# Kernel tuning notes

Measured on AMD Instinct MI355X. Metric: run time of the kernel, lower is better.

The kernel has to match this reference:

```python
import jax, jax.numpy as jnp
import numpy as np

N = 50000        # nodes
E = 300000       # edges (before self-loops)
F_IN = 128       # input feature dim
H = 2            # attention heads
D = 128          # per-head dim (hidden_dim/heads)
C = 3            # output classes
G = 64           # graphs in batch
NEG_SLOPE = 0.2  # PyG GATConv default leaky-relu slope


def setup_inputs() -> dict:
    key = jax.random.key(0)
    ks = jax.random.split(key, 9)
    x = jax.random.normal(ks[0], (N, F_IN), jnp.float32)
    edge_index = jax.random.randint(ks[1], (2, E), 0, N, dtype=jnp.int64)
    batch = jnp.sort(jax.random.randint(ks[2], (N,), 0, G, dtype=jnp.int64))
    W = jax.random.normal(ks[3], (F_IN, H, D), jnp.float32) * 0.05   # GAT lin weight
    att_src = jax.random.normal(ks[4], (H, D), jnp.float32) * 0.1
    att_dst = jax.random.normal(ks[5], (H, D), jnp.float32) * 0.1
    bias_gat = jax.random.normal(ks[6], (H * D,), jnp.float32) * 0.01
    fc_w = jax.random.normal(ks[7], (H * D, C), jnp.float32) * 0.05
    fc_b = jax.random.normal(ks[8], (C,), jnp.float32) * 0.01
    a = jnp.array(1.0, jnp.float32)
    return dict(x=x, edge_index=edge_index, batch=batch, W=W, att_src=att_src,
                att_dst=att_dst, bias_gat=bias_gat, fc_w=fc_w, fc_b=fc_b, a=a)


def reference(x, edge_index, batch, W, att_src, att_dst, bias_gat, fc_w, fc_b, a):
    n = x.shape[0]
    # PyG GATConv adds self-loops by default
    loops = jnp.arange(n, dtype=edge_index.dtype)
    src = jnp.concatenate([edge_index[0], loops])   # message sources j
    tgt = jnp.concatenate([edge_index[1], loops])   # message targets i

    xw = jnp.einsum('nf,nfhd->nhd', x[:, :, None, None] * 0 + x[:, :, None, None], W[None]) if False else jnp.einsum('nf,fhd->nhd', x, W)  # [N,H,D]
    a_s = jnp.sum(xw * att_src, axis=-1)            # [N,H]
    a_d = jnp.sum(xw * att_dst, axis=-1)            # [N,H]

    e = a_s[src] + a_d[tgt]                         # [E+N,H]
    e = jnp.where(e > 0, e, NEG_SLOPE * e)          # leaky relu
    # segment softmax over incoming edges of each target node
    m = jax.ops.segment_max(e, tgt, num_segments=n)
    ex = jnp.exp(e - m[tgt])
    denom = jax.ops.segment_sum(ex, tgt, num_segments=n)
    alpha = ex / denom[tgt]                         # [E+N,H]

    out = jax.ops.segment_sum(alpha[:, :, None] * xw[src], tgt, num_segments=n)  # [N,H,D]
    z = out.reshape(n, H * D) + bias_gat
    z = jax.nn.relu(z)
    z = z @ fc_w + fc_b                              # [N,C]
    z = jax.nn.log_softmax(z, axis=1)
    z = jax.ops.segment_sum(z, batch, num_segments=G)  # global_add_pool -> [G,C]
    z = a * z
    return jax.nn.log_softmax(z, axis=1)
```

## Files before the change

### kernel.cpp

```cpp
#include <hip/hip_runtime.h>
#include <hip/hip_bf16.h>

typedef __hip_bfloat16 bf16;
typedef __attribute__((ext_vector_type(8))) short bf16x8;
typedef __attribute__((ext_vector_type(4))) float f32x4;

#define F_IN    128
#define HD      256
#define N_C     3
#define N_G     64
#define NEG_SLOPE 0.2f
#define NPART   512
#define DMAX    32

__device__ __forceinline__ float b2f(unsigned short u) {
    return __uint_as_float(((unsigned int)u) << 16);
}
__device__ __forceinline__ unsigned short f2bs(float f) {
    unsigned int u = __float_as_uint(f);
    return (unsigned short)((u + 0x7FFFu + ((u >> 16) & 1u)) >> 16);
}

__global__ void scatter_kernel(const int* __restrict__ ei, int* __restrict__ cnt,
                               int* __restrict__ ssrc32,
                               const float* __restrict__ W,
                               unsigned short* __restrict__ WTf, int e) {
    int i = blockIdx.x * blockDim.x + threadIdx.x;
    if (i < HD * F_IN) {
        int j = i & 7;
        int L = (i >> 3) & 63;
        int c = (i >> 9) & 3;
        int t = i >> 11;
        int f  = c * 32 + (L >> 4) * 8 + j;
        int hd = t * 16 + (L & 15);
        WTf[i] = f2bs(W[f * HD + hd]);
    }
    if (i < e) {
        int s = ei[i];
        int t = ei[e + i];
        int p = atomicAdd(&cnt[t], 1);
        if (p < DMAX) ssrc32[(size_t)t * DMAX + p] = s;
    }
}

__global__ __launch_bounds__(256) void xw_mfma_kernel(const float* __restrict__ x,
                                                      const uint4* __restrict__ WTf,
                                                      bf16* __restrict__ xw,
                                                      const float* __restrict__ att_src,
                                                      const float* __restrict__ att_dst,
                                                      float* __restrict__ asd, int n) {
    __shared__ uint4 wt_lds[4096];
    int tid = threadIdx.x;
    int wid = tid >> 6, lane = tid & 63;
    int r16 = lane & 15, quad = lane >> 4;
    int rb = blockIdx.x * 64 + wid * 16;
    bool valid = rb < n;
    int rbl = valid ? rb : 0;

    const float* xr = x + (size_t)(rbl + r16) * F_IN + quad * 8;
    float4 f0a = *(const float4*)(xr + 0);
    float4 f1a = *(const float4*)(xr + 4);
    float4 f0b = *(const float4*)(xr + 32);
    float4 f1b = *(const float4*)(xr + 36);
    float4 f0c = *(const float4*)(xr + 64);
    float4 f1c = *(const float4*)(xr + 68);
    float4 f0d = *(const float4*)(xr + 96);
    float4 f1d = *(const float4*)(xr + 100);

    #pragma unroll
    for (int r = 0; r < 16; r++)
        wt_lds[r * 256 + tid] = WTf[r * 256 + tid];

    bf16x8 xf[4];
    {
        bf16x8 a;
        a[0]=(short)f2bs(f0a.x); a[1]=(short)f2bs(f0a.y); a[2]=(short)f2bs(f0a.z); a[3]=(short)f2bs(f0a.w);
        a[4]=(short)f2bs(f1a.x); a[5]=(short)f2bs(f1a.y); a[6]=(short)f2bs(f1a.z); a[7]=(short)f2bs(f1a.w);
        xf[0]=a;
        a[0]=(short)f2bs(f0b.x); a[1]=(short)f2bs(f0b.y); a[2]=(short)f2bs(f0b.z); a[3]=(short)f2bs(f0b.w);
        a[4]=(short)f2bs(f1b.x); a[5]=(short)f2bs(f1b.y); a[6]=(short)f2bs(f1b.z); a[7]=(short)f2bs(f1b.w);
        xf[1]=a;
        a[0]=(short)f2bs(f0c.x); a[1]=(short)f2bs(f0c.y); a[2]=(short)f2bs(f0c.z); a[3]=(short)f2bs(f0c.w);
        a[4]=(short)f2bs(f1c.x); a[5]=(short)f2bs(f1c.y); a[6]=(short)f2bs(f1c.z); a[7]=(short)f2bs(f1c.w);
        xf[2]=a;
        a[0]=(short)f2bs(f0d.x); a[1]=(short)f2bs(f0d.y); a[2]=(short)f2bs(f0d.z); a[3]=(short)f2bs(f0d.w);
        a[4]=(short)f2bs(f1d.x); a[5]=(short)f2bs(f1d.y); a[6]=(short)f2bs(f1d.z); a[7]=(short)f2bs(f1d.w);
        xf[3]=a;
    }
    __syncthreads();

    const unsigned short* wls = (const unsigned short*)wt_lds;
    float s0a = 0.f, s1a = 0.f, d0a = 0.f, d1a = 0.f;
    for (int t = 0; t < 16; t++) {
        f32x4 acc = {0.f, 0.f, 0.f, 0.f};
        #pragma unroll
        for (int c = 0; c < 4; c++) {
            bf16x8 wf = *(const bf16x8*)(wls + ((t * 4 + c) * 64 + lane) * 8);
            acc = __builtin_amdgcn_mfma_f32_16x16x32_bf16(wf, xf[c], acc, 0, 0, 0);
        }
        int colbase = t * 16;
        float4 as4 = *(const float4*)(att_src + colbase + quad * 4);
        float4 ad4 = *(const float4*)(att_dst + colbase + quad * 4);
        if (valid) {
            unsigned int w0 = (unsigned int)f2bs(acc[0]) | ((unsigned int)f2bs(acc[1]) << 16);
            unsigned int w1 = (unsigned int)f2bs(acc[2]) | ((unsigned int)f2bs(acc[3]) << 16);
            *(uint2*)((unsigned short*)xw + (size_t)(rb + r16) * HD + colbase + quad * 4)
                = make_uint2(w0, w1);
        }
        float ds = acc[0]*as4.x + acc[1]*as4.y + acc[2]*as4.z + acc[3]*as4.w;
        float dd = acc[0]*ad4.x + acc[1]*ad4.y + acc[2]*ad4.z + acc[3]*ad4.w;
        if (t < 8) { s0a += ds; d0a += dd; }
        else       { s1a += ds; d1a += dd; }
    }

    #pragma unroll
    for (int o = 16; o <= 32; o <<= 1) {
        s0a += __shfl_xor(s0a, o, 64);
        s1a += __shfl_xor(s1a, o, 64);
        d0a += __shfl_xor(d0a, o, 64);
        d1a += __shfl_xor(d1a, o, 64);
    }
    if (valid && quad == 0) {
        float4 v;
        v.x = s0a; v.y = s1a; v.z = d0a; v.w = d1a;
        ((float4*)asd)[rb + r16] = v;
    }
}

__global__ __launch_bounds__(256) void main_kernel(const bf16* __restrict__ xw,
                                                   const float* __restrict__ asd,
                                                   const int* __restrict__ cnt,
                                                   const int* __restrict__ ssrc32,
                                                   const int* __restrict__ batch,
                                                   const float* __restrict__ bias,
                                                   const float* __restrict__ fcw,
                                                   const float* __restrict__ fcb,
                                                   float* __restrict__ gsumP, int n) {
    __shared__ int   sidx[4][64];
    __shared__ float salp[4][2][64];
    int wid = threadIdx.x >> 6, lane = threadIdx.x & 63;
    int head = lane >> 5;
    int node = blockIdx.x * 4 + wid;
    if (node >= n) return;

    float4 my = ((const float4*)asd)[node];
    float ad0 = my.z, ad1 = my.w;
    int dege = cnt[node];
    if (dege > DMAX) dege = DMAX;
    int deg = dege + 1;
    const int* srow = ssrc32 + (size_t)node * DMAX;

    float a0 = 0.f, a1 = 0.f, a2 = 0.f, a3 = 0.f;

    bool act = lane < deg;
    int myidx = node;
    float e0 = -1e30f, e1 = -1e30f;
    if (lane < dege) {
        myidx = srow[lane];
        float4 sa = ((const float4*)asd)[myidx];
        e0 = sa.x + ad0;
        e1 = sa.y + ad1;
    } else if (lane == dege) {
        e0 = my.x + ad0;
        e1 = my.y + ad1;
    }
    e0 = (e0 > 0.f) ? e0 : NEG_SLOPE * e0;
    e1 = (e1 > 0.f) ? e1 : NEG_SLOPE * e1;
    if (!act) { e0 = -1e30f; e1 = -1e30f; }

    float m0 = e0, m1 = e1;
    #pragma unroll
    for (int o = 1; o <= 8; o <<= 1) {
        m0 = fmaxf(m0, __shfl_xor(m0, o, 64));
        m1 = fmaxf(m1, __shfl_xor(m1, o, 64));
    }
    if (deg > 16) {
        #pragma unroll
        for (int o = 16; o <= 32; o <<= 1) {
            m0 = fmaxf(m0, __shfl_xor(m0, o, 64));
            m1 = fmaxf(m1, __shfl_xor(m1, o, 64));
        }
    }
    float al0 = act ? __expf(e0 - m0) : 0.f;
    float al1 = act ? __expf(e1 - m1) : 0.f;
    float s0 = al0, s1 = al1;
    #pragma unroll
    for (int o = 1; o <= 8; o <<= 1) {
        s0 += __shfl_xor(s0, o, 64);
        s1 += __shfl_xor(s1, o, 64);
    }
    if (deg > 16) {
        #pragma unroll
        for (int o = 16; o <= 32; o <<= 1) {
            s0 += __shfl_xor(s0, o, 64);
            s1 += __shfl_xor(s1, o, 64);
        }
    }
    if (act) {
        sidx[wid][lane] = myidx;
        salp[wid][0][lane] = al0 / s0;
        salp[wid][1][lane] = al1 / s1;
    }

    int e = 0;
    for (; e + 4 <= deg; e += 4) {
        int i0 = sidx[wid][e + 0], i1 = sidx[wid][e + 1];
        int i2 = sidx[wid][e + 2], i3 = sidx[wid][e + 3];
        ushort4 v0 = ((const ushort4*)(xw + (size_t)i0 * HD))[lane];
        ushort4 v1 = ((const ushort4*)(xw + (size_t)i1 * HD))[lane];
        ushort4 v2 = ((const ushort4*)(xw + (size_t)i2 * HD))[lane];
        ushort4 v3 = ((const ushort4*)(xw + (size_t)i3 * HD))[lane];
        float w0 = salp[wid][head][e + 0];
        float w1 = salp[wid][head][e + 1];
        float w2 = salp[wid][head][e + 2];
        float w3 = salp[wid][head][e + 3];
        a0 += w0 * b2f(v0.x) + w1 * b2f(v1.x) + w2 * b2f(v2.x) + w3 * b2f(v3.x);
        a1 += w0 * b2f(v0.y) + w1 * b2f(v1.y) + w2 * b2f(v2.y) + w3 * b2f(v3.y);
        a2 += w0 * b2f(v0.z) + w1 * b2f(v1.z) + w2 * b2f(v2.z) + w3 * b2f(v3.z);
        a3 += w0 * b2f(v0.w) + w1 * b2f(v1.w) + w2 * b2f(v2.w) + w3 * b2f(v3.w);
    }
    for (; e < deg; e++) {
        int i0 = sidx[wid][e];
        ushort4 v0 = ((const ushort4*)(xw + (size_t)i0 * HD))[lane];
        float w0 = salp[wid][head][e];
        a0 += w0 * b2f(v0.x); a1 += w0 * b2f(v0.y);
        a2 += w0 * b2f(v0.z); a3 += w0 * b2f(v0.w);
    }

    float4 bv = ((const float4*)bias)[lane];
    float z0 = fmaxf(a0 + bv.x, 0.f);
    float z1 = fmaxf(a1 + bv.y, 0.f);
    float z2 = fmaxf(a2 + bv.z, 0.f);
    float z3 = fmaxf(a3 + bv.w, 0.f);

    const float* fp = fcw + lane * 12;
    float4 c0 = *(const float4*)(fp);
    float4 c1 = *(const float4*)(fp + 4);
    float4 c2 = *(const float4*)(fp + 8);
    float l0 = z0 * c0.x + z1 * c0.w + z2 * c1.z + z3 * c2.y;
    float l1 = z0 * c0.y + z1 * c1.x + z2 * c1.w + z3 * c2.z;
    float l2 = z0 * c0.z + z1 * c1.y + z2 * c2.x + z3 * c2.w;
    #pragma unroll
    for (int o = 32; o > 0; o >>= 1) {
        l0 += __shfl_xor(l0, o, 64);
        l1 += __shfl_xor(l1, o, 64);
        l2 += __shfl_xor(l2, o, 64);
    }
    if (lane == 0) {
        l0 += fcb[0]; l1 += fcb[1]; l2 += fcb[2];
        float m = fmaxf(l0, fmaxf(l1, l2));
        float lse = m + __logf(__expf(l0 - m) + __expf(l1 - m) + __expf(l2 - m));
        int b = batch[node];
        int part = node & (NPART - 1);
        atomicAdd(&gsumP[(b * 3 + 0) * NPART + part], l0 - lse);
        atomicAdd(&gsumP[(b * 3 + 1) * NPART + part], l1 - lse);
        atomicAdd(&gsumP[(b * 3 + 2) * NPART + part], l2 - lse);
    }
}

__global__ __launch_bounds__(64) void final_kernel(const float* __restrict__ gsumP,
                                                   const float* __restrict__ a,
                                                   float* __restrict__ out) {
    int g = blockIdx.x;
    int lane = threadIdx.x;
    float v[3];
    #pragma unroll
    for (int c = 0; c < 3; c++) {
        float s = 0.f;
        for (int p = lane; p < NPART; p += 64)
            s += gsumP[(g * 3 + c) * NPART + p];
        #pragma unroll
        for (int o = 32; o > 0; o >>= 1) s += __shfl_xor(s, o, 64);
        v[c] = s;
    }
    if (lane == 0) {
        float av = a[0];
        float v0 = v[0] * av, v1 = v[1] * av, v2 = v[2] * av;
        float m = fmaxf(v0, fmaxf(v1, v2));
        float lse = m + __logf(__expf(v0 - m) + __expf(v1 - m) + __expf(v2 - m));
        out[g * 3 + 0] = v0 - lse;
        out[g * 3 + 1] = v1 - lse;
        out[g * 3 + 2] = v2 - lse;
    }
}

extern "C" void kernel_launch(void* const* d_in, const int* in_sizes, int n_in,
                              void* d_out, int out_size, void* d_ws, size_t ws_size,
                              hipStream_t stream) {
    const float* x       = (const float*)d_in[0];
    const int*   ei      = (const int*)d_in[1];
    const int*   batch   = (const int*)d_in[2];
    const float* W       = (const float*)d_in[3];
    const float* att_src = (const float*)d_in[4];
    const float* att_dst = (const float*)d_in[5];
    const float* bias    = (const float*)d_in[6];
    const float* fcw     = (const float*)d_in[7];
    const float* fcb     = (const float*)d_in[8];
    const float* a_scale = (const float*)d_in[9];
    float* out = (float*)d_out;

    const int n = in_sizes[2];
    const int e = in_sizes[1] / 2;

    char* ws = (char*)d_ws;
    bf16*  xw     = (bf16*)ws;
    float* asd    = (float*)(ws + 25600000);
    int*   cnt    = (int*)(ws + 26400000);
    float* gsumP  = (float*)(ws + 26600000);
    int*   ssrc32 = (int*)(ws + 26993216);
    unsigned short* WTf = (unsigned short*)(ws + 33393216);

    int eb256 = (e + 255) / 256;

    hipMemsetAsync(cnt, 0, (size_t)n * 4 + (size_t)N_G * N_C * NPART * 4, stream);

    hipLaunchKernelGGL(scatter_kernel, dim3(eb256), dim3(256), 0, stream,
                       ei, cnt, ssrc32, W, WTf, e);
    hipLaunchKernelGGL(xw_mfma_kernel, dim3((n + 63) / 64), dim3(256), 0, stream,
                       x, (const uint4*)WTf, xw, att_src, att_dst, asd, n);
    hipLaunchKernelGGL(main_kernel,    dim3((n + 3) / 4), dim3(256), 0, stream,
                       xw, asd, cnt, ssrc32, batch, bias, fcw, fcb, gsumP, n);
    hipLaunchKernelGGL(final_kernel,   dim3(N_G), dim3(64), 0, stream, gsumP, a_scale, out);
}
```

Baseline: 165.9 us.

## Fuse final pooling into main kernel, batch gathers by eight, vectorize edge scatter

```diff
diff --git a/kernel.cpp b/kernel.cpp
--- a/kernel.cpp
+++ b/kernel.cpp
@@ -35,11 +35,16 @@
         int hd = t * 16 + (L & 15);
         WTf[i] = f2bs(W[f * HD + hd]);
     }
-    if (i < e) {
-        int s = ei[i];
-        int t = ei[e + i];
-        int p = atomicAdd(&cnt[t], 1);
-        if (p < DMAX) ssrc32[(size_t)t * DMAX + p] = s;
+    int i2 = i * 2;
+    if (i2 < e) {
+        int2 s2 = *(const int2*)(ei + i2);
+        int2 t2 = *(const int2*)(ei + e + i2);
+        int p = atomicAdd(&cnt[t2.x], 1);
+        if (p < DMAX) ssrc32[(size_t)t2.x * DMAX + p] = s2.x;
+        if (i2 + 1 < e) {
+            p = atomicAdd(&cnt[t2.y], 1);
+            if (p < DMAX) ssrc32[(size_t)t2.y * DMAX + p] = s2.y;
+        }
     }
 }
 
@@ -135,152 +140,154 @@
                                                    const float* __restrict__ bias,
                                                    const float* __restrict__ fcw,
                                                    const float* __restrict__ fcb,
-                                                   float* __restrict__ gsumP, int n) {
+                                                   float* __restrict__ gsumP,
+                                                   const float* __restrict__ a_scale,
+                                                   float* __restrict__ out,
+                                                   int* __restrict__ done, int n) {
     __shared__ int   sidx[4][64];
     __shared__ float salp[4][2][64];
+    __shared__ int   islast;
     int wid = threadIdx.x >> 6, lane = threadIdx.x & 63;
     int head = lane >> 5;
     int node = blockIdx.x * 4 + wid;
-    if (node >= n) return;
-
-    float4 my = ((const float4*)asd)[node];
-    float ad0 = my.z, ad1 = my.w;
-    int dege = cnt[node];
-    if (dege > DMAX) dege = DMAX;
-    int deg = dege + 1;
-    const int* srow = ssrc32 + (size_t)node * DMAX;
-
-    float a0 = 0.f, a1 = 0.f, a2 = 0.f, a3 = 0.f;
-
-    bool act = lane < deg;
-    int myidx = node;
-    float e0 = -1e30f, e1 = -1e30f;
-    if (lane < dege) {
-        myidx = srow[lane];
-        float4 sa = ((const float4*)asd)[myidx];
-        e0 = sa.x + ad0;
-        e1 = sa.y + ad1;
-    } else if (lane == dege) {
-        e0 = my.x + ad0;
-        e1 = my.y + ad1;
-    }
-    e0 = (e0 > 0.f) ? e0 : NEG_SLOPE * e0;
-    e1 = (e1 > 0.f) ? e1 : NEG_SLOPE * e1;
-    if (!act) { e0 = -1e30f; e1 = -1e30f; }
-
-    float m0 = e0, m1 = e1;
-    #pragma unroll
-    for (int o = 1; o <= 8; o <<= 1) {
-        m0 = fmaxf(m0, __shfl_xor(m0, o, 64));
-        m1 = fmaxf(m1, __shfl_xor(m1, o, 64));
-    }
-    if (deg > 16) {
+
+    if (node < n) {
+        float4 my = ((const float4*)asd)[node];
+        float ad0 = my.z, ad1 = my.w;
+        int dege = cnt[node];
+        if (dege > DMAX) dege = DMAX;
+        int deg = dege + 1;
+        const int* srow = ssrc32 + (size_t)node * DMAX;
+
+        float a0 = 0.f, a1 = 0.f, a2 = 0.f, a3 = 0.f;
+
+        bool act = lane < deg;
+        int myidx = node;
+        float e0 = -1e30f, e1 = -1e30f;
+        if (lane < dege) {
+            myidx = srow[lane];
+            float4 sa = ((const float4*)asd)[myidx];
+            e0 = sa.x + ad0;
+            e1 = sa.y + ad1;
+        } else if (lane == dege) {
+            e0 = my.x + ad0;
+            e1 = my.y + ad1;
+        }
+        e0 = (e0 > 0.f) ? e0 : NEG_SLOPE * e0;
+        e1 = (e1 > 0.f) ? e1 : NEG_SLOPE * e1;
+        if (!act) { e0 = -1e30f; e1 = -1e30f; }
+
+        float m0 = e0, m1 = e1;
         #pragma unroll
-        for (int o = 16; o <= 32; o <<= 1) {
+        for (int o = 1; o <= 8; o <<= 1) {
             m0 = fmaxf(m0, __shfl_xor(m0, o, 64));
             m1 = fmaxf(m1, __shfl_xor(m1, o, 64));
         }
-    }
-    float al0 = act ? __expf(e0 - m0) : 0.f;
-    float al1 = act ? __expf(e1 - m1) : 0.f;
-    float s0 = al0, s1 = al1;
-    #pragma unroll
-    for (int o = 1; o <= 8; o <<= 1) {
-        s0 += __shfl_xor(s0, o, 64);
-        s1 += __shfl_xor(s1, o, 64);
-    }
-    if (deg > 16) {
+        if (deg > 16) {
+            #pragma unroll
+            for (int o = 16; o <= 32; o <<= 1) {
+                m0 = fmaxf(m0, __shfl_xor(m0, o, 64));
+                m1 = fmaxf(m1, __shfl_xor(m1, o, 64));
+            }
+        }
+        float al0 = act ? __expf(e0 - m0) : 0.f;
+        float al1 = act ? __expf(e1 - m1) : 0.f;
+        float s0 = al0, s1 = al1;
         #pragma unroll
-        for (int o = 16; o <= 32; o <<= 1) {
+        for (int o = 1; o <= 8; o <<= 1) {
             s0 += __shfl_xor(s0, o, 64);
             s1 += __shfl_xor(s1, o, 64);
         }
-    }
-    if (act) {
+        if (deg > 16) {
+            #pragma unroll
+            for (int o = 16; o <= 32; o <<= 1) {
+                s0 += __shfl_xor(s0, o, 64);
+                s1 += __shfl_xor(s1, o, 64);
+            }
+        }
         sidx[wid][lane] = myidx;
-        salp[wid][0][lane] = al0 / s0;
-        salp[wid][1][lane] = al1 / s1;
-    }
-
-    int e = 0;
-    for (; e + 4 <= deg; e += 4) {
-        int i0 = sidx[wid][e + 0], i1 = sidx[wid][e + 1];
-        int i2 = sidx[wid][e + 2], i3 = sidx[wid][e + 3];
-        ushort4 v0 = ((const ushort4*)(xw + (size_t)i0 * HD))[lane];
-        ushort4 v1 = ((const ushort4*)(xw + (size_t)i1 * HD))[lane];
-        ushort4 v2 = ((const ushort4*)(xw + (size_t)i2 * HD))[lane];
-        ushort4 v3 = ((const ushort4*)(xw + (size_t)i3 * HD))[lane];
-        float w0 = salp[wid][head][e + 0];
-        float w1 = salp[wid][head][e + 1];
-        float w2 = salp[wid][head][e + 2];
-        float w3 = salp[wid][head][e + 3];
-        a0 += w0 * b2f(v0.x) + w1 * b2f(v1.x) + w2 * b2f(v2.x) + w3 * b2f(v3.x);
-        a1 += w0 * b2f(v0.y) + w1 * b2f(v1.y) + w2 * b2f(v2.y) + w3 * b2f(v3.y);
-        a2 += w0 * b2f(v0.z) + w1 * b2f(v1.z) + w2 * b2f(v2.z) + w3 * b2f(v3.z);
-        a3 += w0 * b2f(v0.w) + w1 * b2f(v1.w) + w2 * b2f(v2.w) + w3 * b2f(v3.w);
-    }
-    for (; e < deg; e++) {
-        int i0 = sidx[wid][e];
-        ushort4 v0 = ((const ushort4*)(xw + (size_t)i0 * HD))[lane];
-        float w0 = salp[wid][head][e];
-        a0 += w0 * b2f(v0.x); a1 += w0 * b2f(v0.y);
-        a2 += w0 * b2f(v0.z); a3 += w0 * b2f(v0.w);
-    }
-
-    float4 bv = ((const float4*)bias)[lane];
-    float z0 = fmaxf(a0 + bv.x, 0.f);
-    float z1 = fmaxf(a1 + bv.y, 0.f);
-    float z2 = fmaxf(a2 + bv.z, 0.f);
-    float z3 = fmaxf(a3 + bv.w, 0.f);
-
-    const float* fp = fcw + lane * 12;
-    float4 c0 = *(const float4*)(fp);
-    float4 c1 = *(const float4*)(fp + 4);
-    float4 c2 = *(const float4*)(fp + 8);
-    float l0 = z0 * c0.x + z1 * c0.w + z2 * c1.z + z3 * c2.y;
-    float l1 = z0 * c0.y + z1 * c1.x + z2 * c1.w + z3 * c2.z;
-    float l2 = z0 * c0.z + z1 * c1.y + z2 * c2.x + z3 * c2.w;
-    #pragma unroll
-    for (int o = 32; o > 0; o >>= 1) {
-        l0 += __shfl_xor(l0, o, 64);
-        l1 += __shfl_xor(l1, o, 64);
-        l2 += __shfl_xor(l2, o, 64);
-    }
-    if (lane == 0) {
-        l0 += fcb[0]; l1 += fcb[1]; l2 += fcb[2];
-        float m = fmaxf(l0, fmaxf(l1, l2));
-        float lse = m + __logf(__expf(l0 - m) + __expf(l1 - m) + __expf(l2 - m));
-        int b = batch[node];
-        int part = node & (NPART - 1);
-        atomicAdd(&gsumP[(b * 3 + 0) * NPART + part], l0 - lse);
-        atomicAdd(&gsumP[(b * 3 + 1) * NPART + part], l1 - lse);
-        atomicAdd(&gsumP[(b * 3 + 2) * NPART + part], l2 - lse);
-    }
-}
-
-__global__ __launch_bounds__(64) void final_kernel(const float* __restrict__ gsumP,
-                                                   const float* __restrict__ a,
-                                                   float* __restrict__ out) {
-    int g = blockIdx.x;
-    int lane = threadIdx.x;
-    float v[3];
-    #pragma unroll
-    for (int c = 0; c < 3; c++) {
-        float s = 0.f;
-        for (int p = lane; p < NPART; p += 64)
-            s += gsumP[(g * 3 + c) * NPART + p];
+        salp[wid][0][lane] = act ? al0 / s0 : 0.f;
+        salp[wid][1][lane] = act ? al1 / s1 : 0.f;
+
+        int nb = (deg + 7) >> 3;
+        for (int b = 0; b < nb; b++) {
+            int eb = b * 8;
+            int idx[8]; ushort4 v[8]; float w[8];
+            #pragma unroll
+            for (int k = 0; k < 8; k++) idx[k] = sidx[wid][eb + k];
+            #pragma unroll
+            for (int k = 0; k < 8; k++)
+                v[k] = ((const ushort4*)(xw + (size_t)idx[k] * HD))[lane];
+            #pragma unroll
+            for (int k = 0; k < 8; k++) w[k] = salp[wid][head][eb + k];
+            #pragma unroll
+            for (int k = 0; k < 8; k++) {
+                a0 += w[k] * b2f(v[k].x); a1 += w[k] * b2f(v[k].y);
+                a2 += w[k] * b2f(v[k].z); a3 += w[k] * b2f(v[k].w);
+            }
+        }
+
+        float4 bv = ((const float4*)bias)[lane];
+        float z0 = fmaxf(a0 + bv.x, 0.f);
+        float z1 = fmaxf(a1 + bv.y, 0.f);
+        float z2 = fmaxf(a2 + bv.z, 0.f);
+        float z3 = fmaxf(a3 + bv.w, 0.f);
+
+        const float* fp = fcw + lane * 12;
+        float4 c0 = *(const float4*)(fp);
+        float4 c1 = *(const float4*)(fp + 4);
+        float4 c2 = *(const float4*)(fp + 8);
+        float l0 = z0 * c0.x + z1 * c0.w + z2 * c1.z + z3 * c2.y;
+        float l1 = z0 * c0.y + z1 * c1.x + z2 * c1.w + z3 * c2.z;
+        float l2 = z0 * c0.z + z1 * c1.y + z2 * c2.x + z3 * c2.w;
         #pragma unroll
-        for (int o = 32; o > 0; o >>= 1) s += __shfl_xor(s, o, 64);
-        v[c] = s;
-    }
-    if (lane == 0) {
-        float av = a[0];
-        float v0 = v[0] * av, v1 = v[1] * av, v2 = v[2] * av;
-        float m = fmaxf(v0, fmaxf(v1, v2));
-        float lse = m + __logf(__expf(v0 - m) + __expf(v1 - m) + __expf(v2 - m));
-        out[g * 3 + 0] = v0 - lse;
-        out[g * 3 + 1] = v1 - lse;
-        out[g * 3 + 2] = v2 - lse;
+        for (int o = 32; o > 0; o >>= 1) {
+            l0 += __shfl_xor(l0, o, 64);
+            l1 += __shfl_xor(l1, o, 64);
+            l2 += __shfl_xor(l2, o, 64);
+        }
+        if (lane == 0) {
+            l0 += fcb[0]; l1 += fcb[1]; l2 += fcb[2];
+            float m = fmaxf(l0, fmaxf(l1, l2));
+            float lse = m + __logf(__expf(l0 - m) + __expf(l1 - m) + __expf(l2 - m));
+            int b = batch[node];
+            int part = node & (NPART - 1);
+            atomicAdd(&gsumP[(b * 3 + 0) * NPART + part], l0 - lse);
+            atomicAdd(&gsumP[(b * 3 + 1) * NPART + part], l1 - lse);
+            atomicAdd(&gsumP[(b * 3 + 2) * NPART + part], l2 - lse);
+        }
+    }
+
+    __syncthreads();
+    if (threadIdx.x == 0) {
+        __threadfence();
+        int t = atomicAdd(done, 1);
+        islast = (t == (int)gridDim.x - 1);
+    }
+    __syncthreads();
+    if (islast) {
+        __threadfence();
+        int tid = threadIdx.x;
+        if (tid < N_G) {
+            float v[3];
+            #pragma unroll
+            for (int c = 0; c < 3; c++) {
+                float s = 0.f;
+                const float4* p4 = (const float4*)(gsumP + (size_t)(tid * 3 + c) * NPART);
+                for (int p = 0; p < NPART / 4; p++) {
+                    float4 q = p4[p];
+                    s += q.x + q.y + q.z + q.w;
+                }
+                v[c] = s;
+            }
+            float av = a_scale[0];
+            float v0 = v[0] * av, v1 = v[1] * av, v2 = v[2] * av;
+            float m = fmaxf(v0, fmaxf(v1, v2));
+            float lse = m + __logf(__expf(v0 - m) + __expf(v1 - m) + __expf(v2 - m));
+            out[tid * 3 + 0] = v0 - lse;
+            out[tid * 3 + 1] = v1 - lse;
+            out[tid * 3 + 2] = v2 - lse;
+        }
     }
 }
 
@@ -307,18 +314,18 @@
     float* asd    = (float*)(ws + 25600000);
     int*   cnt    = (int*)(ws + 26400000);
     float* gsumP  = (float*)(ws + 26600000);
-    int*   ssrc32 = (int*)(ws + 26993216);
-    unsigned short* WTf = (unsigned short*)(ws + 33393216);
-
-    int eb256 = (e + 255) / 256;
-
-    hipMemsetAsync(cnt, 0, (size_t)n * 4 + (size_t)N_G * N_C * NPART * 4, stream);
-
+    int*   done   = (int*)(ws + 26993216);
+    int*   ssrc32 = (int*)(ws + 26993280);
+    unsigned short* WTf = (unsigned short*)(ws + 33393280);
+
+    hipMemsetAsync(cnt, 0, (size_t)n * 4 + (size_t)N_G * N_C * NPART * 4 + 64, stream);
+
+    int eb256 = (e / 2 + 255) / 256;
     hipLaunchKernelGGL(scatter_kernel, dim3(eb256), dim3(256), 0, stream,
                        ei, cnt, ssrc32, W, WTf, e);
     hipLaunchKernelGGL(xw_mfma_kernel, dim3((n + 63) / 64), dim3(256), 0, stream,
                        x, (const uint4*)WTf, xw, att_src, att_dst, asd, n);
     hipLaunchKernelGGL(main_kernel,    dim3((n + 3) / 4), dim3(256), 0, stream,
-                       xw, asd, cnt, ssrc32, batch, bias, fcw, fcb, gsumP, n);
-    hipLaunchKernelGGL(final_kernel,   dim3(N_G), dim3(64), 0, stream, gsumP, a_scale, out);
-}
+                       xw, asd, cnt, ssrc32, batch, bias, fcw, fcb, gsumP,
+                       a_scale, out, done, n);
+}
```

New measurement: 505.4 us. 3.05x slower.
